# Optimization experiments

Measured on AMD Instinct MI355X. Metric: run time of the kernel, lower is better.

Reference implementation:

```python
import jax, jax.numpy as jnp
import numpy as np
import math

F, M, C, OUT = 60, 600, 8, 18  # feature_size, max_samples, cluster_size, output_dim
B = 2048


def l2_normalize(x, axis):
    # matches tf.nn.l2_normalize (epsilon=1e-12)
    sq = jnp.sum(jnp.square(x), axis=axis, keepdims=True)
    return x * jax.lax.rsqrt(jnp.maximum(sq, 1e-12))


def setup_inputs() -> dict:
    key = jax.random.key(0)
    k = jax.random.split(key, 6)
    s1 = 1.0 / math.sqrt(F)
    s2 = 1.0 / math.sqrt(C)
    return {
        "reshaped_input": jax.random.normal(k[0], (B * M, F), dtype=jnp.float32),
        "cluster_weights": jax.random.normal(k[1], (F, C), dtype=jnp.float32) * s1,
        "covar_weights": jax.random.normal(k[2], (F, C), dtype=jnp.float32) * s1,
        "cluster_biases": jax.random.normal(k[3], (C,), dtype=jnp.float32) * s1,
        "cluster_weights2": jax.random.normal(k[4], (1, F, C), dtype=jnp.float32) * s1,
        "hidden1_weights": jax.random.normal(k[5], (2 * C * F, OUT), dtype=jnp.float32) * s2,
    }


def reference(reshaped_input, cluster_weights, covar_weights, cluster_biases,
              cluster_weights2, hidden1_weights):
    cw = jnp.square(covar_weights) + 1e-6                      # [F, C]

    act = reshaped_input @ cluster_weights + cluster_biases    # [B*M, C]
    act = jax.nn.softmax(act, axis=-1)
    act = act.reshape(-1, M, C)                                # [B, M, C]

    a_sum = jnp.sum(act, axis=-2, keepdims=True)               # [B, 1, C]
    a = a_sum * cluster_weights2                               # [B, F, C]

    x = reshaped_input.reshape(-1, M, F)                       # [B, M, F]

    fv1 = jnp.einsum('bmc,bmf->bfc', act, x)                   # [B, F, C]
    fv2 = jnp.einsum('bmc,bmf->bfc', act, jnp.square(x))       # [B, F, C]

    a2 = a_sum * jnp.square(cluster_weights2)                  # [B, F, C]
    b2 = fv1 * cluster_weights2                                # [B, F, C]

    fv2 = a2 + fv2 - 2.0 * b2
    fv2 = fv2 / jnp.square(cw)
    fv2 = fv2 - a_sum                                          # broadcast [B,1,C]
    fv2 = fv2.reshape(-1, C * F)
    fv2 = l2_normalize(fv2, axis=1)
    fv2 = l2_normalize(fv2, axis=1)  # second normalize as in original (idempotent)

    fv1 = (fv1 - a) / cw                                       # [B, F, C]
    fv1 = l2_normalize(fv1, axis=1)                            # per-cluster, along F
    fv1 = fv1.reshape(-1, C * F)
    fv1 = l2_normalize(fv1, axis=1)

    fv = jnp.concatenate([fv1, fv2], axis=1)                   # [B, 2*C*F]
    return fv @ hidden1_weights                                # [B, OUT]
```

## Files before the change

### kernel.cpp

```cpp
#include <hip/hip_runtime.h>

#define FDIM 60
#define MROW 600
#define CDIM 8
#define ODIM 18
#define CH   128
#define NCHUNK 5
#define BLK  512

typedef short bf16x8 __attribute__((ext_vector_type(8)));
typedef float f32x4  __attribute__((ext_vector_type(4)));

__device__ __forceinline__ unsigned int packrne2(float lo, float hi) {
    unsigned int ul = __float_as_uint(lo), uh = __float_as_uint(hi);
    ul = (ul + 0x7fffu + ((ul >> 16) & 1u)) >> 16;
    uh = (uh + 0x7fffu + ((uh >> 16) & 1u)) & 0xffff0000u;
    return (ul & 0xffffu) | uh;
}

__global__ void __launch_bounds__(BLK, 4) netfv_kernel(
    const float* __restrict__ x,
    const float* __restrict__ W,
    const float* __restrict__ covar,
    const float* __restrict__ bias,
    const float* __restrict__ cw2,
    const float* __restrict__ H,
    float* __restrict__ out)
{
    __shared__ __align__(16) short xsT1[64 * 136];
    __shared__ __align__(16) short xsT2[64 * 136];
    __shared__ __align__(16) short actT[16 * 136];
    __shared__ __align__(16) float Wt[8 * 64];
    __shared__ __align__(16) float fvbuf[1024];
    __shared__ __align__(16) float fvl[960];
    __shared__ float redA[64], redB[64];
    __shared__ float asuml[8], n1rs[8], n1c_s[8], n2c_s[8], scal[2];

    const int tid  = threadIdx.x;
    const int b    = blockIdx.x;
    const int lane = tid & 63;
    const int wv   = tid >> 6;
    const int mg   = tid >> 3;
    const int fs   = tid & 7;

    { int c = tid >> 6, f = tid & 63; Wt[c * 64 + f] = (f < FDIM) ? W[f * 8 + c] : 0.f; }
    {
        unsigned int* az = (unsigned int*)(actT + 8 * 136);
        for (int i = tid; i < 544; i += BLK) az[i] = 0u;
    }
    float bl[8];
    #pragma unroll
    for (int c = 0; c < 8; ++c) bl[c] = bias[c];

    const int fvsel = wv & 1;
    const int tile  = wv >> 1;
    const int ln15  = lane & 15;
    const int quad  = lane >> 4;
    f32x4 acc = {0.f, 0.f, 0.f, 0.f};
    float asum_l = 0.f;

    __syncthreads();

    const size_t rowbase = (size_t)b * (MROW * FDIM);

    for (int ck = 0; ck < NCHUNK; ++ck) {
        const int r0  = 2 * mg;
        const int r0g = ck * CH + r0;
        const bool valid = (r0g < MROW);

        float xv0[8], xv1[8];
        float act0 = 0.f, act1 = 0.f;
        if (valid) {
            const float* p0 = x + rowbase + (size_t)r0g * FDIM + 8 * fs;
            const float* p1 = p0 + FDIM;
            float4 A0 = *(const float4*)p0;
            float4 A1 = *(const float4*)p1;
            float4 B0 = {0.f,0.f,0.f,0.f}, B1 = {0.f,0.f,0.f,0.f};
            if (fs < 7) { B0 = *(const float4*)(p0 + 4); B1 = *(const float4*)(p1 + 4); }
            xv0[0]=A0.x; xv0[1]=A0.y; xv0[2]=A0.z; xv0[3]=A0.w;
            xv0[4]=B0.x; xv0[5]=B0.y; xv0[6]=B0.z; xv0[7]=B0.w;
            xv1[0]=A1.x; xv1[1]=A1.y; xv1[2]=A1.z; xv1[3]=A1.w;
            xv1[4]=B1.x; xv1[5]=B1.y; xv1[6]=B1.z; xv1[7]=B1.w;

            float lg0[8], lg1[8];
            #pragma unroll
            for (int c = 0; c < 8; ++c) {
                float4 w0 = *(const float4*)&Wt[c * 64 + 8 * fs];
                float4 w1 = *(const float4*)&Wt[c * 64 + 8 * fs + 4];
                float s0 = 0.f, s1 = 0.f;
                s0 = fmaf(xv0[0], w0.x, s0); s0 = fmaf(xv0[1], w0.y, s0);
                s0 = fmaf(xv0[2], w0.z, s0); s0 = fmaf(xv0[3], w0.w, s0);
                s0 = fmaf(xv0[4], w1.x, s0); s0 = fmaf(xv0[5], w1.y, s0);
                s0 = fmaf(xv0[6], w1.z, s0); s0 = fmaf(xv0[7], w1.w, s0);
                s1 = fmaf(xv1[0], w0.x, s1); s1 = fmaf(xv1[1], w0.y, s1);
                s1 = fmaf(xv1[2], w0.z, s1); s1 = fmaf(xv1[3], w0.w, s1);
                s1 = fmaf(xv1[4], w1.x, s1); s1 = fmaf(xv1[5], w1.y, s1);
                s1 = fmaf(xv1[6], w1.z, s1); s1 = fmaf(xv1[7], w1.w, s1);
                lg0[c] = s0; lg1[c] = s1;
            }
            #pragma unroll
            for (int c = 0; c < 8; ++c) {
                lg0[c] += __shfl_xor(lg0[c], 1);
                lg0[c] += __shfl_xor(lg0[c], 2);
                lg0[c] += __shfl_xor(lg0[c], 4);
                lg1[c] += __shfl_xor(lg1[c], 1);
                lg1[c] += __shfl_xor(lg1[c], 2);
                lg1[c] += __shfl_xor(lg1[c], 4);
                lg0[c] += bl[c]; lg1[c] += bl[c];
            }
            float mx0 = lg0[0], mx1 = lg1[0];
            #pragma unroll
            for (int c = 1; c < 8; ++c) { mx0 = fmaxf(mx0, lg0[c]); mx1 = fmaxf(mx1, lg1[c]); }
            float s0 = 0.f, s1 = 0.f;
            #pragma unroll
            for (int c = 0; c < 8; ++c) {
                lg0[c] = __expf(lg0[c] - mx0); s0 += lg0[c];
                lg1[c] = __expf(lg1[c] - mx1); s1 += lg1[c];
            }
            float i0 = 1.f / s0, i1 = 1.f / s1;
            #pragma unroll
            for (int c = 0; c < 8; ++c)
                if (c == fs) { act0 = lg0[c] * i0; act1 = lg1[c] * i1; }
            asum_l += act0 + act1;
        }
        ((unsigned int*)actT)[fs * 68 + mg] = valid ? packrne2(act0, act1) : 0u;
        if (valid) {
            const int wbase = (((mg >> 2) ^ fs) << 2) + (mg & 3);
            #pragma unroll
            for (int i = 0; i < 8; ++i) {
                int f = 8 * fs + i;
                int woff = f * 68 + wbase;
                ((unsigned int*)xsT1)[woff] = packrne2(xv0[i], xv1[i]);
                ((unsigned int*)xsT2)[woff] = packrne2(xv0[i] * xv0[i], xv1[i] * xv1[i]);
            }
        }
        __syncthreads();

        {
            const short* xsel = fvsel ? xsT2 : xsT1;
            const int f   = tile * 16 + ln15;
            const int fsw = f >> 3;
            #pragma unroll
            for (int ks = 0; ks < 4; ++ks) {
                bf16x8 av = *(const bf16x8*)(actT + ln15 * 136 + ks * 32 + quad * 8);
                int kblk = ks * 4 + quad;
                bf16x8 bv = *(const bf16x8*)(xsel + f * 136 + ((kblk ^ fsw) << 3));
                acc = __builtin_amdgcn_mfma_f32_16x16x32_bf16(av, bv, acc, 0, 0, 0);
            }
        }
        __syncthreads();
    }

    {
        float v = asum_l;
        v += __shfl_down(v, 8); v += __shfl_down(v, 16); v += __shfl_down(v, 32);
        if (lane < 8) redA[wv * 8 + lane] = v;
    }
    __syncthreads();
    if (tid < 64) {
        float v = redA[tid];
        v += __shfl_down(v, 8); v += __shfl_down(v, 16); v += __shfl_down(v, 32);
        if (tid < 8) asuml[tid] = v;
    }
    if (quad < 2) {
        #pragma unroll
        for (int r = 0; r < 4; ++r) {
            int c = quad * 4 + r;
            int f = tile * 16 + ln15;
            fvbuf[fvsel * 512 + f * 8 + c] = acc[r];
        }
    }
    __syncthreads();

    float fv1v = 0.f, fv2v = 0.f;
    const int f_e = tid >> 3, c_e = tid & 7;
    if (tid < 480) {
        float fv1r = fvbuf[f_e * 8 + c_e];
        float fv2r = fvbuf[512 + f_e * 8 + c_e];
        float asv  = asuml[c_e];
        float cw2v = cw2[f_e * 8 + c_e];
        float cv   = covar[f_e * 8 + c_e];
        float cwv  = cv * cv + 1e-6f;
        float rcw  = 1.0f / cwv;
        fv1v = (fv1r - asv * cw2v) * rcw;
        fv2v = (fmaf(asv * cw2v, cw2v, fv2r) - 2.0f * fv1r * cw2v) * rcw * rcw - asv;
    }

    {
        float p1 = fv1v * fv1v, p2 = fv2v * fv2v;
        p1 += __shfl_down(p1, 8);  p2 += __shfl_down(p2, 8);
        p1 += __shfl_down(p1, 16); p2 += __shfl_down(p2, 16);
        p1 += __shfl_down(p1, 32); p2 += __shfl_down(p2, 32);
        if (lane < 8) { redA[wv * 8 + lane] = p1; redB[wv * 8 + lane] = p2; }
    }
    __syncthreads();
    if (tid < 64) {
        float q1 = redA[tid], q2 = redB[tid];
        q1 += __shfl_down(q1, 8);  q2 += __shfl_down(q2, 8);
        q1 += __shfl_down(q1, 16); q2 += __shfl_down(q2, 16);
        q1 += __shfl_down(q1, 32); q2 += __shfl_down(q2, 32);
        if (tid < 8) { n1c_s[tid] = q1; n2c_s[tid] = q2; }
    }
    __syncthreads();
    if (tid == 0) {
        float S1 = 0.f, S2 = 0.f;
        #pragma unroll
        for (int c = 0; c < 8; ++c) {
            float rs = rsqrtf(fmaxf(n1c_s[c], 1e-12f));
            n1rs[c] = rs;
            S1 += n1c_s[c] * rs * rs;
            S2 += n2c_s[c];
        }
        scal[0] = rsqrtf(fmaxf(S1, 1e-12f));
        scal[1] = rsqrtf(fmaxf(S2, 1e-12f));
    }
    __syncthreads();
    if (tid < 480) {
        fvl[f_e * 8 + c_e]       = fv1v * n1rs[c_e] * scal[0];
        fvl[480 + f_e * 8 + c_e] = fv2v * scal[1];
    }
    __syncthreads();

    for (int o = wv; o < ODIM; o += 8) {
        float sacc = 0.f;
        #pragma unroll 5
        for (int i = lane; i < 960; i += 64)
            sacc = fmaf(fvl[i], H[i * ODIM + o], sacc);
        sacc += __shfl_down(sacc, 32);
        sacc += __shfl_down(sacc, 16);
        sacc += __shfl_down(sacc, 8);
        sacc += __shfl_down(sacc, 4);
        sacc += __shfl_down(sacc, 2);
        sacc += __shfl_down(sacc, 1);
        if (lane == 0) out[(size_t)b * ODIM + o] = sacc;
    }
}

extern "C" void kernel_launch(void* const* d_in, const int* in_sizes, int n_in,
                              void* d_out, int out_size, void* d_ws, size_t ws_size,
                              hipStream_t stream) {
    const float* x     = (const float*)d_in[0];
    const float* W     = (const float*)d_in[1];
    const float* covar = (const float*)d_in[2];
    const float* bias  = (const float*)d_in[3];
    const float* cw2   = (const float*)d_in[4];
    const float* H     = (const float*)d_in[5];
    float* outp = (float*)d_out;

    const int Bn = in_sizes[0] / (MROW * FDIM);
    hipLaunchKernelGGL(netfv_kernel, dim3(Bn), dim3(BLK), 0, stream,
                       x, W, covar, bias, cw2, H, outp);
}
```

Baseline: 440.5 us.

## Compute cluster logits with MFMA and prefetch next chunk of rows

Cluster logits are now computed with bf16 MFMA on a row-major bf16 copy of the input tile, replacing the scalar FMA loop and xor-shuffle reductions, and softmax is done per MFMA output layout. Global loads for the next chunk are issued before processing the current one, overlapping memory latency with compute. This adds an extra shared-memory buffer, an extra barrier per chunk, bf16 rounding of the logits, and higher register use from the prefetched float4s.

```diff
diff --git a/kernel.cpp b/kernel.cpp
--- a/kernel.cpp
+++ b/kernel.cpp
@@ -11,11 +11,16 @@
 typedef short bf16x8 __attribute__((ext_vector_type(8)));
 typedef float f32x4  __attribute__((ext_vector_type(4)));
 
-__device__ __forceinline__ unsigned int packrne2(float lo, float hi) {
+__device__ __forceinline__ unsigned int pk2(float lo, float hi) {
     unsigned int ul = __float_as_uint(lo), uh = __float_as_uint(hi);
     ul = (ul + 0x7fffu + ((ul >> 16) & 1u)) >> 16;
     uh = (uh + 0x7fffu + ((uh >> 16) & 1u)) & 0xffff0000u;
     return (ul & 0xffffu) | uh;
+}
+__device__ __forceinline__ short f2bf(float f) {
+    unsigned int u = __float_as_uint(f);
+    u = (u + 0x7fffu + ((u >> 16) & 1u)) >> 16;
+    return (short)u;
 }
 
 __global__ void __launch_bounds__(BLK, 4) netfv_kernel(
@@ -29,8 +34,9 @@
 {
     __shared__ __align__(16) short xsT1[64 * 136];
     __shared__ __align__(16) short xsT2[64 * 136];
+    __shared__ __align__(16) short xsM [128 * 72];
     __shared__ __align__(16) short actT[16 * 136];
-    __shared__ __align__(16) float Wt[8 * 64];
+    __shared__ __align__(16) short WtB [16 * 72];
     __shared__ __align__(16) float fvbuf[1024];
     __shared__ __align__(16) float fvl[960];
     __shared__ float redA[64], redB[64];
@@ -42,96 +48,99 @@
     const int wv   = tid >> 6;
     const int mg   = tid >> 3;
     const int fs   = tid & 7;
-
-    { int c = tid >> 6, f = tid & 63; Wt[c * 64 + f] = (f < FDIM) ? W[f * 8 + c] : 0.f; }
+    const int ln15 = lane & 15;
+    const int quad = lane >> 4;
+    const int fvsel = wv & 1;
+    const int tile  = wv >> 1;
+
+    const size_t rowbase = (size_t)b * (MROW * FDIM);
+    const float* prow = x + rowbase + (size_t)(2 * mg) * FDIM + 8 * fs;
+
+    float4 A0, A1, B0, B1;
+    B0 = B1 = make_float4(0.f, 0.f, 0.f, 0.f);
+    A0 = *(const float4*)prow;
+    A1 = *(const float4*)(prow + FDIM);
+    if (fs < 7) { B0 = *(const float4*)(prow + 4); B1 = *(const float4*)(prow + FDIM + 4); }
+
+    if (tid < 512) {
+        int c = tid >> 5, j = tid & 31;
+        float v0 = (2 * j     < FDIM) ? W[(2 * j) * CDIM + c % CDIM]     : 0.f;
+        float v1 = (2 * j + 1 < FDIM) ? W[(2 * j + 1) * CDIM + c % CDIM] : 0.f;
+        if (c >= CDIM) { v0 = 0.f; v1 = 0.f; }
+        ((unsigned int*)WtB)[c * 36 + j] = pk2(v0, v1);
+    }
     {
         unsigned int* az = (unsigned int*)(actT + 8 * 136);
         for (int i = tid; i < 544; i += BLK) az[i] = 0u;
     }
-    float bl[8];
-    #pragma unroll
-    for (int c = 0; c < 8; ++c) bl[c] = bias[c];
-
-    const int fvsel = wv & 1;
-    const int tile  = wv >> 1;
-    const int ln15  = lane & 15;
-    const int quad  = lane >> 4;
+    __syncthreads();
+
+    const bf16x8 aw0 = *(const bf16x8*)(WtB + ln15 * 72 + quad * 8);
+    const bf16x8 aw1 = *(const bf16x8*)(WtB + ln15 * 72 + 32 + quad * 8);
+    const float4 lb  = *(const float4*)(bias + (quad & 1) * 4);
+
     f32x4 acc = {0.f, 0.f, 0.f, 0.f};
-    float asum_l = 0.f;
-
-    __syncthreads();
-
-    const size_t rowbase = (size_t)b * (MROW * FDIM);
+    float asum_acc[4] = {0.f, 0.f, 0.f, 0.f};
+    const int mloc = wv * 16 + ln15;
 
     for (int ck = 0; ck < NCHUNK; ++ck) {
-        const int r0  = 2 * mg;
-        const int r0g = ck * CH + r0;
-        const bool valid = (r0g < MROW);
-
-        float xv0[8], xv1[8];
-        float act0 = 0.f, act1 = 0.f;
+        const bool valid = (ck * CH + 2 * mg) < MROW;
+
+        float4 nA0, nA1, nB0, nB1;
+        nA0 = nA1 = nB0 = nB1 = make_float4(0.f, 0.f, 0.f, 0.f);
+        if (ck + 1 < NCHUNK && ((ck + 1) * CH + 2 * mg) < MROW) {
+            const float* pn = prow + (size_t)(ck + 1) * (CH * FDIM);
+            nA0 = *(const float4*)pn;
+            nA1 = *(const float4*)(pn + FDIM);
+            if (fs < 7) { nB0 = *(const float4*)(pn + 4); nB1 = *(const float4*)(pn + FDIM + 4); }
+        }
+
         if (valid) {
-            const float* p0 = x + rowbase + (size_t)r0g * FDIM + 8 * fs;
-            const float* p1 = p0 + FDIM;
-            float4 A0 = *(const float4*)p0;
-            float4 A1 = *(const float4*)p1;
-            float4 B0 = {0.f,0.f,0.f,0.f}, B1 = {0.f,0.f,0.f,0.f};
-            if (fs < 7) { B0 = *(const float4*)(p0 + 4); B1 = *(const float4*)(p1 + 4); }
-            xv0[0]=A0.x; xv0[1]=A0.y; xv0[2]=A0.z; xv0[3]=A0.w;
-            xv0[4]=B0.x; xv0[5]=B0.y; xv0[6]=B0.z; xv0[7]=B0.w;
-            xv1[0]=A1.x; xv1[1]=A1.y; xv1[2]=A1.z; xv1[3]=A1.w;
-            xv1[4]=B1.x; xv1[5]=B1.y; xv1[6]=B1.z; xv1[7]=B1.w;
-
-            float lg0[8], lg1[8];
-            #pragma unroll
-            for (int c = 0; c < 8; ++c) {
-                float4 w0 = *(const float4*)&Wt[c * 64 + 8 * fs];
-                float4 w1 = *(const float4*)&Wt[c * 64 + 8 * fs + 4];
-                float s0 = 0.f, s1 = 0.f;
-                s0 = fmaf(xv0[0], w0.x, s0); s0 = fmaf(xv0[1], w0.y, s0);
-                s0 = fmaf(xv0[2], w0.z, s0); s0 = fmaf(xv0[3], w0.w, s0);
-                s0 = fmaf(xv0[4], w1.x, s0); s0 = fmaf(xv0[5], w1.y, s0);
-                s0 = fmaf(xv0[6], w1.z, s0); s0 = fmaf(xv0[7], w1.w, s0);
-                s1 = fmaf(xv1[0], w0.x, s1); s1 = fmaf(xv1[1], w0.y, s1);
-                s1 = fmaf(xv1[2], w0.z, s1); s1 = fmaf(xv1[3], w0.w, s1);
-                s1 = fmaf(xv1[4], w1.x, s1); s1 = fmaf(xv1[5], w1.y, s1);
-                s1 = fmaf(xv1[6], w1.z, s1); s1 = fmaf(xv1[7], w1.w, s1);
-                lg0[c] = s0; lg1[c] = s1;
-            }
-            #pragma unroll
-            for (int c = 0; c < 8; ++c) {
-                lg0[c] += __shfl_xor(lg0[c], 1);
-                lg0[c] += __shfl_xor(lg0[c], 2);
-                lg0[c] += __shfl_xor(lg0[c], 4);
-                lg1[c] += __shfl_xor(lg1[c], 1);
-                lg1[c] += __shfl_xor(lg1[c], 2);
-                lg1[c] += __shfl_xor(lg1[c], 4);
-                lg0[c] += bl[c]; lg1[c] += bl[c];
-            }
-            float mx0 = lg0[0], mx1 = lg1[0];
-            #pragma unroll
-            for (int c = 1; c < 8; ++c) { mx0 = fmaxf(mx0, lg0[c]); mx1 = fmaxf(mx1, lg1[c]); }
-            float s0 = 0.f, s1 = 0.f;
-            #pragma unroll
-            for (int c = 0; c < 8; ++c) {
-                lg0[c] = __expf(lg0[c] - mx0); s0 += lg0[c];
-                lg1[c] = __expf(lg1[c] - mx1); s1 += lg1[c];
-            }
-            float i0 = 1.f / s0, i1 = 1.f / s1;
-            #pragma unroll
-            for (int c = 0; c < 8; ++c)
-                if (c == fs) { act0 = lg0[c] * i0; act1 = lg1[c] * i1; }
-            asum_l += act0 + act1;
-        }
-        ((unsigned int*)actT)[fs * 68 + mg] = valid ? packrne2(act0, act1) : 0u;
-        if (valid) {
+            float xv0[8] = {A0.x, A0.y, A0.z, A0.w, B0.x, B0.y, B0.z, B0.w};
+            float xv1[8] = {A1.x, A1.y, A1.z, A1.w, B1.x, B1.y, B1.z, B1.w};
+            {
+                unsigned int q0 = pk2(xv0[0], xv0[1]), q1 = pk2(xv0[2], xv0[3]);
+                unsigned int q2 = pk2(xv0[4], xv0[5]), q3 = pk2(xv0[6], xv0[7]);
+                *(uint4*)(xsM + (2 * mg) * 72 + 8 * fs) = make_uint4(q0, q1, q2, q3);
+                unsigned int s0 = pk2(xv1[0], xv1[1]), s1 = pk2(xv1[2], xv1[3]);
+                unsigned int s2 = pk2(xv1[4], xv1[5]), s3 = pk2(xv1[6], xv1[7]);
+                *(uint4*)(xsM + (2 * mg + 1) * 72 + 8 * fs) = make_uint4(s0, s1, s2, s3);
+            }
             const int wbase = (((mg >> 2) ^ fs) << 2) + (mg & 3);
             #pragma unroll
             for (int i = 0; i < 8; ++i) {
-                int f = 8 * fs + i;
-                int woff = f * 68 + wbase;
-                ((unsigned int*)xsT1)[woff] = packrne2(xv0[i], xv1[i]);
-                ((unsigned int*)xsT2)[woff] = packrne2(xv0[i] * xv0[i], xv1[i] * xv1[i]);
+                int woff = (8 * fs + i) * 68 + wbase;
+                ((unsigned int*)xsT1)[woff] = pk2(xv0[i], xv1[i]);
+                ((unsigned int*)xsT2)[woff] = pk2(xv0[i] * xv0[i], xv1[i] * xv1[i]);
+            }
+        }
+        __syncthreads();
+
+        {
+            bf16x8 bv0 = *(const bf16x8*)(xsM + mloc * 72 + quad * 8);
+            bf16x8 bv1 = *(const bf16x8*)(xsM + mloc * 72 + 32 + quad * 8);
+            f32x4 lz = {0.f, 0.f, 0.f, 0.f};
+            lz = __builtin_amdgcn_mfma_f32_16x16x32_bf16(aw0, bv0, lz, 0, 0, 0);
+            lz = __builtin_amdgcn_mfma_f32_16x16x32_bf16(aw1, bv1, lz, 0, 0, 0);
+            float L0 = lz[0] + lb.x, L1 = lz[1] + lb.y;
+            float L2 = lz[2] + lb.z, L3 = lz[3] + lb.w;
+            float mx = fmaxf(fmaxf(L0, L1), fmaxf(L2, L3));
+            mx = fmaxf(mx, __shfl_xor(mx, 16));
+            float e0 = __expf(L0 - mx), e1 = __expf(L1 - mx);
+            float e2 = __expf(L2 - mx), e3 = __expf(L3 - mx);
+            float s = e0 + e1 + e2 + e3;
+            s += __shfl_xor(s, 16);
+            float inv = __builtin_amdgcn_rcpf(s);
+            const bool vm = (ck * CH + mloc) < MROW;
+            if (quad < 2) {
+                float a0 = vm ? e0 * inv : 0.f, a1v = vm ? e1 * inv : 0.f;
+                float a2v = vm ? e2 * inv : 0.f, a3v = vm ? e3 * inv : 0.f;
+                asum_acc[0] += a0;  asum_acc[1] += a1v;
+                asum_acc[2] += a2v; asum_acc[3] += a3v;
+                actT[(quad * 4 + 0) * 136 + mloc] = f2bf(a0);
+                actT[(quad * 4 + 1) * 136 + mloc] = f2bf(a1v);
+                actT[(quad * 4 + 2) * 136 + mloc] = f2bf(a2v);
+                actT[(quad * 4 + 3) * 136 + mloc] = f2bf(a3v);
             }
         }
         __syncthreads();
@@ -149,12 +158,19 @@
             }
         }
         __syncthreads();
-    }
-
-    {
-        float v = asum_l;
-        v += __shfl_down(v, 8); v += __shfl_down(v, 16); v += __shfl_down(v, 32);
-        if (lane < 8) redA[wv * 8 + lane] = v;
+        A0 = nA0; A1 = nA1; B0 = nB0; B1 = nB1;
+    }
+
+    #pragma unroll
+    for (int r = 0; r < 4; ++r) {
+        float v = asum_acc[r];
+        v += __shfl_xor(v, 1); v += __shfl_xor(v, 2);
+        v += __shfl_xor(v, 4); v += __shfl_xor(v, 8);
+        asum_acc[r] = v;
+    }
+    if (quad < 2 && ln15 == 0) {
+        #pragma unroll
+        for (int r = 0; r < 4; ++r) redA[wv * 8 + quad * 4 + r] = asum_acc[r];
     }
     __syncthreads();
     if (tid < 64) {
@@ -164,11 +180,8 @@
     }
     if (quad < 2) {
         #pragma unroll
-        for (int r = 0; r < 4; ++r) {
-            int c = quad * 4 + r;
-            int f = tile * 16 + ln15;
-            fvbuf[fvsel * 512 + f * 8 + c] = acc[r];
-        }
+        for (int r = 0; r < 4; ++r)
+            fvbuf[fvsel * 512 + (tile * 16 + ln15) * 8 + quad * 4 + r] = acc[r];
     }
     __syncthreads();
 
```

After: 440.3 us. About the same (-0.1%).
